# Kernel optimization log

Measured on AMD Instinct MI355X. Metric: run time of the kernel, lower is better.

The kernel has to match this reference:

```python
import jax, jax.numpy as jnp
import numpy as np

B, S, D, H = 4, 2048, 1024, 16
HD = D // H  # 64


def setup_inputs() -> dict:
    key = jax.random.key(0)
    k1, k2, k3 = jax.random.split(key, 3)
    scale = 1.0 / np.sqrt(D)
    return {
        "x": jax.random.normal(k1, (B, S, D), dtype=jnp.float32),
        "W_qkv": jax.random.normal(k2, (3 * D, D), dtype=jnp.float32) * scale,
        "b_qkv": jnp.zeros((3 * D,), dtype=jnp.float32),
        "W_out": jax.random.normal(k3, (D, D), dtype=jnp.float32) * scale,
        "b_out": jnp.zeros((D,), dtype=jnp.float32),
    }


def reference(x, W_qkv, b_qkv, W_out, b_out):
    b, s, d = x.shape
    # fused QKV projection: [b, s, 3d]
    qkv = jnp.einsum("bsd,ed->bse", x, W_qkv) + b_qkv
    # [b, s, H, 3*hd] -> [b, H, s, 3*hd]
    qkv = qkv.reshape(b, s, H, 3 * HD).transpose(0, 2, 1, 3)
    q, k, v = jnp.split(qkv, 3, axis=-1)  # each [b, H, s, hd]
    scaled = jnp.einsum("bhqd,bhkd->bhqk", q, k) / jnp.sqrt(jnp.float32(HD))
    attention = jax.nn.softmax(scaled, axis=-1)  # [b, H, s, s]
    values = jnp.einsum("bhqk,bhkd->bhqd", attention, v)
    values = values.transpose(0, 2, 1, 3).reshape(b, s, d)
    out = jnp.einsum("bsd,ed->bse", values, W_out) + b_out
    return out
```

## Files before the change

### kernel.cpp

```cpp
#include <hip/hip_runtime.h>

#define SEQ   2048
#define DM    1024
#define NHEAD 16
#define NBAT  4
#define NQKV  3072
#define MTOT  8192

typedef __attribute__((ext_vector_type(8))) short bf16x8;
typedef __attribute__((ext_vector_type(4))) float f32x4;
typedef __attribute__((ext_vector_type(16))) float f32x16;
typedef __attribute__((ext_vector_type(2))) unsigned int uint2v;

__device__ __forceinline__ unsigned short f2bf(float f) {
    union { float f; unsigned int u; } v; v.f = f;
    return (unsigned short)((v.u + 0x7FFFu + ((v.u >> 16) & 1u)) >> 16);
}

__device__ __forceinline__ void gl_lds16(const void* g, void* l) {
    __builtin_amdgcn_global_load_lds(
        (const __attribute__((address_space(1))) unsigned int*)(unsigned long long)g,
        (__attribute__((address_space(3))) unsigned int*)(unsigned int)(unsigned long long)l,
        16, 0, 0);
}

__global__ __launch_bounds__(256) void k_cvt_all(const float* __restrict__ x,
                                                 const float* __restrict__ wq,
                                                 const float* __restrict__ wo,
                                                 unsigned short* __restrict__ xb,
                                                 unsigned short* __restrict__ wqb,
                                                 unsigned short* __restrict__ wob) {
    int i = blockIdx.x * 256 + threadIdx.x;
    const float* s; unsigned short* d; int j;
    if (i < 2097152)      { s = x;  d = xb;  j = i; }
    else if (i < 2883584) { s = wq; d = wqb; j = i - 2097152; }
    else                  { s = wo; d = wob; j = i - 2883584; }
    float4 v = reinterpret_cast<const float4*>(s)[j];
    ushort4 o = { f2bf(v.x), f2bf(v.y), f2bf(v.z), f2bf(v.w) };
    reinterpret_cast<ushort4*>(d)[j] = o;
}

__global__ __launch_bounds__(256) void k_qkv(const unsigned short* __restrict__ X,
                                             const unsigned short* __restrict__ W,
                                             const float* __restrict__ bias,
                                             unsigned short* __restrict__ Qb,
                                             unsigned short* __restrict__ Kb,
                                             unsigned short* __restrict__ Vtb) {
    __shared__ short As[2][128 * 32];
    __shared__ short Bs[2][128 * 32];

    const int tid = threadIdx.x;
    const int lane = tid & 63;
    const int wid = tid >> 6;
    const int lr = lane & 15, g = lane >> 4;
    const int lb = (blockIdx.x & 7) * 192 + (blockIdx.x >> 3);
    const int bm = lb / (NQKV / 128);
    const int bn = lb % (NQKV / 128);
    const int m0 = bm * 128, n0 = bn * 128;
    const int wr = (wid >> 1) * 64, wc = (wid & 1) * 64;

    const f32x4 fz = {0.f, 0.f, 0.f, 0.f};
    f32x4 acc[4][4];
#pragma unroll
    for (int i = 0; i < 4; ++i)
#pragma unroll
        for (int j = 0; j < 4; ++j) acc[i][j] = fz;

    auto stage = [&](int buf, int kt) {
#pragma unroll
        for (int p = 0; p < 2; ++p) {
            int c = wid * 128 + p * 64 + lane;
            int r_ = c >> 2;
            int kc = (c & 3) ^ (r_ & 3);
            gl_lds16(X + (size_t)(m0 + r_) * DM + kt * 32 + kc * 8, &As[buf][c * 8]);
            gl_lds16(W + (size_t)(n0 + r_) * DM + kt * 32 + kc * 8, &Bs[buf][c * 8]);
        }
    };

    stage(0, 0);
    __syncthreads();

    for (int kt = 0; kt < 32; ++kt) {
        const int cur = kt & 1;
        if (kt + 1 < 32) stage(cur ^ 1, kt + 1);
        bf16x8 a[4], b[4];
#pragma unroll
        for (int i = 0; i < 4; ++i) {
            int ra = wr + i * 16 + lr;
            a[i] = *(const bf16x8*)&As[cur][ra * 32 + ((g ^ (ra & 3)) * 8)];
            int rb = wc + i * 16 + lr;
            b[i] = *(const bf16x8*)&Bs[cur][rb * 32 + ((g ^ (rb & 3)) * 8)];
        }
#pragma unroll
        for (int i = 0; i < 4; ++i)
#pragma unroll
            for (int j = 0; j < 4; ++j)
                acc[i][j] = __builtin_amdgcn_mfma_f32_16x16x32_bf16(a[i], b[j], acc[i][j], 0, 0, 0);
        __syncthreads();
    }

#pragma unroll
    for (int j = 0; j < 4; ++j) {
        const int col = n0 + wc + j * 16 + lr;
        const int h = col / 192;
        const int cc = col - h * 192;
        const int part = cc >> 6;
        const int hd = cc & 63;
        const float bv = bias[col];
#pragma unroll
        for (int i = 0; i < 4; ++i) {
            const int mbase = m0 + wr + i * 16 + g * 4;
            const int b_ = mbase >> 11;
            const int s_ = mbase & 2047;
            const int bh = b_ * NHEAD + h;
            if (part == 2) {
                ushort4 pk = { f2bf(acc[i][j][0] + bv), f2bf(acc[i][j][1] + bv),
                               f2bf(acc[i][j][2] + bv), f2bf(acc[i][j][3] + bv) };
                *(ushort4*)&Vtb[((size_t)bh * 64 + hd) * SEQ + s_] = pk;
            } else {
#pragma unroll
                for (int r = 0; r < 4; ++r) {
                    const size_t idx = ((size_t)bh * SEQ + s_ + r) * 64 + hd;
                    float v = acc[i][j][r] + bv;
                    if (part == 0) Qb[idx] = f2bf(v * (0.125f * 1.44269504f));
                    else           Kb[idx] = f2bf(v);
                }
            }
        }
    }
}

__global__ __launch_bounds__(256) void k_attn(const unsigned short* __restrict__ Qb,
                                              const unsigned short* __restrict__ Kb,
                                              const unsigned short* __restrict__ Vtb,
                                              unsigned short* __restrict__ Ob) {
    __shared__ short Ks[2][64 * 64];
    __shared__ short Vs[2][64 * 64];

    const int tid = threadIdx.x;
    const int lane = tid & 63;
    const int wid = tid >> 6;
    const int lb = (blockIdx.x & 7) * 128 + (blockIdx.x >> 3);
    const int bh = lb >> 4;
    const int qt = lb & 15;
    const int c = lane & 31;
    const int hi = lane >> 5;

    const unsigned short* Qh = Qb + (size_t)bh * SEQ * 64;
    const unsigned short* Kh = Kb + (size_t)bh * SEQ * 64;
    const unsigned short* Vh = Vtb + (size_t)bh * 64 * SEQ;

    const int q0 = qt * 128 + wid * 32;

    bf16x8 qf[4];
#pragma unroll
    for (int kc = 0; kc < 4; ++kc)
        qf[kc] = *(const bf16x8*)&Qh[(size_t)(q0 + c) * 64 + kc * 16 + hi * 8];

    f32x16 oacc[2];
    f32x16 lacc;
    f32x16 fz16;
#pragma unroll
    for (int r = 0; r < 16; ++r) { oacc[0][r] = 0.f; oacc[1][r] = 0.f; lacc[r] = 0.f; fz16[r] = 0.f; }

    auto stageK = [&](int buf, int kt) {
#pragma unroll
        for (int p = 0; p < 2; ++p) {
            int ci = wid * 128 + p * 64 + lane;
            int r_ = ci >> 3;
            int kc = (ci & 7) ^ (r_ & 7);
            gl_lds16(Kh + (size_t)(kt * 64 + r_) * 64 + kc * 8, &Ks[buf][ci * 8]);
        }
    };
    auto stageV = [&](int buf, int kt) {
#pragma unroll
        for (int p = 0; p < 2; ++p) {
            int ci = wid * 128 + p * 64 + lane;
            int r_ = ci >> 3;
            int kc = (ci & 7) ^ (r_ & 7);
            gl_lds16(Vh + (size_t)r_ * SEQ + kt * 64 + kc * 8, &Vs[buf][ci * 8]);
        }
    };

    stageK(0, 0);
    stageV(0, 0);
    __syncthreads();

    auto tile = [&](int cur, int kt) {
        if (kt + 1 < 32) { stageK(cur ^ 1, kt + 1); stageV(cur ^ 1, kt + 1); }

        f32x16 st[2];
        __builtin_amdgcn_s_setprio(1);
#pragma unroll
        for (int t = 0; t < 2; ++t) {
            const int row = t * 32 + c;
            bf16x8 kf0 = *(const bf16x8*)&Ks[cur][row * 64 + (((hi) ^ (row & 7)) * 8)];
            st[t] = __builtin_amdgcn_mfma_f32_32x32x16_bf16(kf0, qf[0], fz16, 0, 0, 0);
#pragma unroll
            for (int kc = 1; kc < 4; ++kc) {
                bf16x8 kf = *(const bf16x8*)&Ks[cur][row * 64 + (((kc * 2 + hi) ^ (row & 7)) * 8)];
                st[t] = __builtin_amdgcn_mfma_f32_32x32x16_bf16(kf, qf[kc], st[t], 0, 0, 0);
            }
        }
        __builtin_amdgcn_s_setprio(0);

#pragma unroll
        for (int t = 0; t < 2; ++t)
#pragma unroll
            for (int r = 0; r < 16; ++r)
                st[t][r] = __builtin_amdgcn_exp2f(st[t][r]);
#pragma unroll
        for (int r = 0; r < 16; ++r)
            lacc[r] += st[0][r] + st[1][r];

        bf16x8 pa[4];
#pragma unroll
        for (int t = 0; t < 2; ++t) {
            unsigned int qd[8];
#pragma unroll
            for (int i = 0; i < 8; ++i) {
                float lo = st[t][2 * i], hg = st[t][2 * i + 1];
                unsigned int d;
                asm("v_cvt_pk_bf16_f32 %0, %1, %2" : "=v"(d) : "v"(lo), "v"(hg));
                qd[i] = d;
            }
            uint2v s02 = __builtin_amdgcn_permlane32_swap(qd[0], qd[2], false, false);
            uint2v s13 = __builtin_amdgcn_permlane32_swap(qd[1], qd[3], false, false);
            uint2v s46 = __builtin_amdgcn_permlane32_swap(qd[4], qd[6], false, false);
            uint2v s57 = __builtin_amdgcn_permlane32_swap(qd[5], qd[7], false, false);
            union { unsigned int u[4]; bf16x8 v; } pk0, pk1;
            pk0.u[0] = s02.x; pk0.u[1] = s13.x; pk0.u[2] = s02.y; pk0.u[3] = s13.y;
            pk1.u[0] = s46.x; pk1.u[1] = s57.x; pk1.u[2] = s46.y; pk1.u[3] = s57.y;
            pa[t * 2] = pk0.v;
            pa[t * 2 + 1] = pk1.v;
        }

        __builtin_amdgcn_s_setprio(1);
#pragma unroll
        for (int nb = 0; nb < 2; ++nb) {
            const int row = nb * 32 + c;
#pragma unroll
            for (int ks = 0; ks < 4; ++ks) {
                bf16x8 vf = *(const bf16x8*)&Vs[cur][row * 64 + (((ks * 2 + hi) ^ (row & 7)) * 8)];
                oacc[nb] = __builtin_amdgcn_mfma_f32_32x32x16_bf16(pa[ks], vf, oacc[nb], 0, 0, 0);
            }
        }
        __builtin_amdgcn_s_setprio(0);

        __syncthreads();
    };

    for (int kt = 0; kt < 32; kt += 2) { tile(0, kt); tile(1, kt + 1); }

    float lred[16];
#pragma unroll
    for (int r = 0; r < 16; ++r) lred[r] = lacc[r];
#pragma unroll
    for (int s2 = 8; s2 > 0; s2 >>= 1)
#pragma unroll
        for (int r = 0; r < s2; ++r) lred[r] += lred[r + s2];
    const float l_all = lred[0] + __shfl_xor(lred[0], 32);

    const int b_ = bh >> 4, h_ = bh & 15;
    const float linv = 1.0f / l_all;
#pragma unroll
    for (int r = 0; r < 16; ++r) {
        const int qrow = (r & 3) + 8 * (r >> 2) + 4 * hi;
        const float fr = __shfl(linv, qrow);
        const size_t mrow = (size_t)b_ * SEQ + q0 + qrow;
#pragma unroll
        for (int nb = 0; nb < 2; ++nb)
            Ob[mrow * DM + h_ * 64 + nb * 32 + c] = f2bf(oacc[nb][r] * fr);
    }
}

__global__ __launch_bounds__(256) void k_out(const unsigned short* __restrict__ A,
                                             const unsigned short* __restrict__ W,
                                             const float* __restrict__ bias,
                                             float* __restrict__ O) {
    __shared__ short As[2][128 * 32];
    __shared__ short Bs[2][128 * 32];

    const int tid = threadIdx.x;
    const int lane = tid & 63;
    const int wid = tid >> 6;
    const int lr = lane & 15, g = lane >> 4;
    const int lb = (blockIdx.x & 7) * 64 + (blockIdx.x >> 3);
    const int bm = lb / (DM / 128);
    const int bn = lb % (DM / 128);
    const int m0 = bm * 128, n0 = bn * 128;
    const int wr = (wid >> 1) * 64, wc = (wid & 1) * 64;

    const f32x4 fz = {0.f, 0.f, 0.f, 0.f};
    f32x4 acc[4][4];
#pragma unroll
    for (int i = 0; i < 4; ++i)
#pragma unroll
        for (int j = 0; j < 4; ++j) acc[i][j] = fz;

    auto stage = [&](int buf, int kt) {
#pragma unroll
        for (int p = 0; p < 2; ++p) {
            int c = wid * 128 + p * 64 + lane;
            int r_ = c >> 2;
            int kc = (c & 3) ^ (r_ & 3);
            gl_lds16(A + (size_t)(m0 + r_) * DM + kt * 32 + kc * 8, &As[buf][c * 8]);
            gl_lds16(W + (size_t)(n0 + r_) * DM + kt * 32 + kc * 8, &Bs[buf][c * 8]);
        }
    };

    stage(0, 0);
    __syncthreads();

    for (int kt = 0; kt < 32; ++kt) {
        const int cur = kt & 1;
        if (kt + 1 < 32) stage(cur ^ 1, kt + 1);
        bf16x8 a[4], b[4];
#pragma unroll
        for (int i = 0; i < 4; ++i) {
            int ra = wr + i * 16 + lr;
            a[i] = *(const bf16x8*)&As[cur][ra * 32 + ((g ^ (ra & 3)) * 8)];
            int rb = wc + i * 16 + lr;
            b[i] = *(const bf16x8*)&Bs[cur][rb * 32 + ((g ^ (rb & 3)) * 8)];
        }
#pragma unroll
        for (int i = 0; i < 4; ++i)
#pragma unroll
            for (int j = 0; j < 4; ++j)
                acc[i][j] = __builtin_amdgcn_mfma_f32_16x16x32_bf16(a[i], b[j], acc[i][j], 0, 0, 0);
        __syncthreads();
    }

#pragma unroll
    for (int j = 0; j < 4; ++j) {
        const int col = n0 + wc + j * 16 + lr;
        const float bv = bias[col];
#pragma unroll
        for (int i = 0; i < 4; ++i) {
            const int mb = m0 + wr + i * 16 + g * 4;
#pragma unroll
            for (int r = 0; r < 4; ++r)
                O[(size_t)(mb + r) * DM + col] = acc[i][j][r] + bv;
        }
    }
}

extern "C" void kernel_launch(void* const* d_in, const int* in_sizes, int n_in,
                              void* d_out, int out_size, void* d_ws, size_t ws_size,
                              hipStream_t stream) {
    const float* x    = (const float*)d_in[0];
    const float* Wqkv = (const float*)d_in[1];
    const float* bqkv = (const float*)d_in[2];
    const float* Wout = (const float*)d_in[3];
    const float* bout = (const float*)d_in[4];
    float* out = (float*)d_out;

    char* ws = (char*)d_ws;
    unsigned short* xb   = (unsigned short*)(ws);
    unsigned short* wqb  = (unsigned short*)(ws + (16u << 20));
    unsigned short* wob  = (unsigned short*)(ws + (22u << 20));
    unsigned short* Qb   = (unsigned short*)(ws + (24u << 20));
    unsigned short* Kb   = (unsigned short*)(ws + (40u << 20));
    unsigned short* Vtb  = (unsigned short*)(ws + (56u << 20));
    unsigned short* valb = (unsigned short*)(ws + (72u << 20));

    k_cvt_all<<<12288, 256, 0, stream>>>(x, Wqkv, Wout, xb, wqb, wob);
    k_qkv<<<64 * 24, 256, 0, stream>>>(xb, wqb, bqkv, Qb, Kb, Vtb);
    k_attn<<<64 * 16, 256, 0, stream>>>(Qb, Kb, Vtb, valb);
    k_out<<<64 * 8, 256, 0, stream>>>(valb, wob, bout, out);
}
```

Measured before the change: 202.4 us.

## Load K and V fragments directly from global memory instead of LDS staging

Removes the double-buffered LDS staging of K and V tiles, along with the per-tile barriers, in the attention kernel. Each wave now loads its MFMA operand fragments for K and transposed V straight from global memory into registers, and the two MFMA chains are interleaved. This drops LDS traffic and synchronisation, but each of the four waves now fetches the same K/V data separately and relies on cache hits. Load latency is also no longer hidden by the prefetch of the next tile.

```diff
diff --git a/kernel.cpp b/kernel.cpp
--- a/kernel.cpp
+++ b/kernel.cpp
@@ -134,9 +134,6 @@
                                               const unsigned short* __restrict__ Kb,
                                               const unsigned short* __restrict__ Vtb,
                                               unsigned short* __restrict__ Ob) {
-    __shared__ short Ks[2][64 * 64];
-    __shared__ short Vs[2][64 * 64];
-
     const int tid = threadIdx.x;
     const int lane = tid & 63;
     const int wid = tid >> 6;
@@ -163,46 +160,35 @@
 #pragma unroll
     for (int r = 0; r < 16; ++r) { oacc[0][r] = 0.f; oacc[1][r] = 0.f; lacc[r] = 0.f; fz16[r] = 0.f; }
 
-    auto stageK = [&](int buf, int kt) {
-#pragma unroll
-        for (int p = 0; p < 2; ++p) {
-            int ci = wid * 128 + p * 64 + lane;
-            int r_ = ci >> 3;
-            int kc = (ci & 7) ^ (r_ & 7);
-            gl_lds16(Kh + (size_t)(kt * 64 + r_) * 64 + kc * 8, &Ks[buf][ci * 8]);
-        }
-    };
-    auto stageV = [&](int buf, int kt) {
-#pragma unroll
-        for (int p = 0; p < 2; ++p) {
-            int ci = wid * 128 + p * 64 + lane;
-            int r_ = ci >> 3;
-            int kc = (ci & 7) ^ (r_ & 7);
-            gl_lds16(Vh + (size_t)r_ * SEQ + kt * 64 + kc * 8, &Vs[buf][ci * 8]);
-        }
-    };
-
-    stageK(0, 0);
-    stageV(0, 0);
-    __syncthreads();
-
-    auto tile = [&](int cur, int kt) {
-        if (kt + 1 < 32) { stageK(cur ^ 1, kt + 1); stageV(cur ^ 1, kt + 1); }
+    const unsigned short* kp = Kh + (size_t)c * 64 + hi * 8;
+    const unsigned short* vp0 = Vh + (size_t)c * SEQ + hi * 8;
+    const unsigned short* vp1 = Vh + (size_t)(32 + c) * SEQ + hi * 8;
+
+    for (int kt = 0; kt < 32; ++kt) {
+        bf16x8 kf0[4], kf1[4];
+#pragma unroll
+        for (int kc = 0; kc < 4; ++kc) {
+            kf0[kc] = *(const bf16x8*)&kp[(size_t)kt * 4096 + kc * 16];
+            kf1[kc] = *(const bf16x8*)&kp[(size_t)kt * 4096 + 2048 + kc * 16];
+        }
 
         f32x16 st[2];
         __builtin_amdgcn_s_setprio(1);
-#pragma unroll
-        for (int t = 0; t < 2; ++t) {
-            const int row = t * 32 + c;
-            bf16x8 kf0 = *(const bf16x8*)&Ks[cur][row * 64 + (((hi) ^ (row & 7)) * 8)];
-            st[t] = __builtin_amdgcn_mfma_f32_32x32x16_bf16(kf0, qf[0], fz16, 0, 0, 0);
-#pragma unroll
-            for (int kc = 1; kc < 4; ++kc) {
-                bf16x8 kf = *(const bf16x8*)&Ks[cur][row * 64 + (((kc * 2 + hi) ^ (row & 7)) * 8)];
-                st[t] = __builtin_amdgcn_mfma_f32_32x32x16_bf16(kf, qf[kc], st[t], 0, 0, 0);
-            }
+        st[0] = __builtin_amdgcn_mfma_f32_32x32x16_bf16(kf0[0], qf[0], fz16, 0, 0, 0);
+        st[1] = __builtin_amdgcn_mfma_f32_32x32x16_bf16(kf1[0], qf[0], fz16, 0, 0, 0);
+#pragma unroll
+        for (int kc = 1; kc < 4; ++kc) {
+            st[0] = __builtin_amdgcn_mfma_f32_32x32x16_bf16(kf0[kc], qf[kc], st[0], 0, 0, 0);
+            st[1] = __builtin_amdgcn_mfma_f32_32x32x16_bf16(kf1[kc], qf[kc], st[1], 0, 0, 0);
         }
         __builtin_amdgcn_s_setprio(0);
+
+        bf16x8 vf0[4], vf1[4];
+#pragma unroll
+        for (int ks = 0; ks < 4; ++ks) {
+            vf0[ks] = *(const bf16x8*)&vp0[kt * 64 + ks * 16];
+            vf1[ks] = *(const bf16x8*)&vp1[kt * 64 + ks * 16];
+        }
 
 #pragma unroll
         for (int t = 0; t < 2; ++t)
@@ -237,20 +223,12 @@
 
         __builtin_amdgcn_s_setprio(1);
 #pragma unroll
-        for (int nb = 0; nb < 2; ++nb) {
-            const int row = nb * 32 + c;
-#pragma unroll
-            for (int ks = 0; ks < 4; ++ks) {
-                bf16x8 vf = *(const bf16x8*)&Vs[cur][row * 64 + (((ks * 2 + hi) ^ (row & 7)) * 8)];
-                oacc[nb] = __builtin_amdgcn_mfma_f32_32x32x16_bf16(pa[ks], vf, oacc[nb], 0, 0, 0);
-            }
+        for (int ks = 0; ks < 4; ++ks) {
+            oacc[0] = __builtin_amdgcn_mfma_f32_32x32x16_bf16(pa[ks], vf0[ks], oacc[0], 0, 0, 0);
+            oacc[1] = __builtin_amdgcn_mfma_f32_32x32x16_bf16(pa[ks], vf1[ks], oacc[1], 0, 0, 0);
         }
         __builtin_amdgcn_s_setprio(0);
-
-        __syncthreads();
-    };
-
-    for (int kt = 0; kt < 32; kt += 2) { tile(0, kt); tile(1, kt + 1); }
+    }
 
     float lred[16];
 #pragma unroll
```

Result: slower. 343.2 us (+69.6%).

## Prefetch GEMM tiles two stages ahead and hoist V fragment loads in attention

Applied to the files above, without the earlier changes.

Both projection GEMMs now issue global-to-LDS loads two k-tiles ahead. They use explicit vmcnt waits and split barriers, so the next stage is issued after fragments are read into registers rather than before the MFMAs. This is meant to hide global load latency better and to drop the trailing full __syncthreads per iteration. In the attention kernel, the V fragments are read from LDS before the exp and pack phase, so LDS latency overlaps the softmax math. The cost is higher register pressure and reliance on hand-counted vmcnt values being correct.

```diff
diff --git a/kernel.cpp b/kernel.cpp
--- a/kernel.cpp
+++ b/kernel.cpp
@@ -78,11 +78,14 @@
     };
 
     stage(0, 0);
-    __syncthreads();
+    stage(1, 1);
 
     for (int kt = 0; kt < 32; ++kt) {
         const int cur = kt & 1;
-        if (kt + 1 < 32) stage(cur ^ 1, kt + 1);
+        if (kt < 31) asm volatile("s_waitcnt vmcnt(4)" ::: "memory");
+        else         asm volatile("s_waitcnt vmcnt(0)" ::: "memory");
+        __builtin_amdgcn_s_barrier();
+
         bf16x8 a[4], b[4];
 #pragma unroll
         for (int i = 0; i < 4; ++i) {
@@ -91,12 +94,16 @@
             int rb = wc + i * 16 + lr;
             b[i] = *(const bf16x8*)&Bs[cur][rb * 32 + ((g ^ (rb & 3)) * 8)];
         }
+        asm volatile("s_waitcnt lgkmcnt(0)" ::: "memory");
+        __builtin_amdgcn_sched_barrier(0);
+        __builtin_amdgcn_s_barrier();
+        if (kt + 2 < 32) stage(cur, kt + 2);
+
 #pragma unroll
         for (int i = 0; i < 4; ++i)
 #pragma unroll
             for (int j = 0; j < 4; ++j)
                 acc[i][j] = __builtin_amdgcn_mfma_f32_16x16x32_bf16(a[i], b[j], acc[i][j], 0, 0, 0);
-        __syncthreads();
     }
 
 #pragma unroll
@@ -203,6 +210,15 @@
             }
         }
         __builtin_amdgcn_s_setprio(0);
+
+        bf16x8 vf[2][4];
+#pragma unroll
+        for (int nb = 0; nb < 2; ++nb) {
+            const int row = nb * 32 + c;
+#pragma unroll
+            for (int ks = 0; ks < 4; ++ks)
+                vf[nb][ks] = *(const bf16x8*)&Vs[cur][row * 64 + (((ks * 2 + hi) ^ (row & 7)) * 8)];
+        }
 
 #pragma unroll
         for (int t = 0; t < 2; ++t)
@@ -237,13 +253,9 @@
 
         __builtin_amdgcn_s_setprio(1);
 #pragma unroll
-        for (int nb = 0; nb < 2; ++nb) {
-            const int row = nb * 32 + c;
-#pragma unroll
-            for (int ks = 0; ks < 4; ++ks) {
-                bf16x8 vf = *(const bf16x8*)&Vs[cur][row * 64 + (((ks * 2 + hi) ^ (row & 7)) * 8)];
-                oacc[nb] = __builtin_amdgcn_mfma_f32_32x32x16_bf16(pa[ks], vf, oacc[nb], 0, 0, 0);
-            }
+        for (int ks = 0; ks < 4; ++ks) {
+            oacc[0] = __builtin_amdgcn_mfma_f32_32x32x16_bf16(pa[ks], vf[0][ks], oacc[0], 0, 0, 0);
+            oacc[1] = __builtin_amdgcn_mfma_f32_32x32x16_bf16(pa[ks], vf[1][ks], oacc[1], 0, 0, 0);
         }
         __builtin_amdgcn_s_setprio(0);
 
@@ -310,11 +322,14 @@
     };
 
     stage(0, 0);
-    __syncthreads();
+    stage(1, 1);
 
     for (int kt = 0; kt < 32; ++kt) {
         const int cur = kt & 1;
-        if (kt + 1 < 32) stage(cur ^ 1, kt + 1);
+        if (kt < 31) asm volatile("s_waitcnt vmcnt(4)" ::: "memory");
+        else         asm volatile("s_waitcnt vmcnt(0)" ::: "memory");
+        __builtin_amdgcn_s_barrier();
+
         bf16x8 a[4], b[4];
 #pragma unroll
         for (int i = 0; i < 4; ++i) {
@@ -323,12 +338,16 @@
             int rb = wc + i * 16 + lr;
             b[i] = *(const bf16x8*)&Bs[cur][rb * 32 + ((g ^ (rb & 3)) * 8)];
         }
+        asm volatile("s_waitcnt lgkmcnt(0)" ::: "memory");
+        __builtin_amdgcn_sched_barrier(0);
+        __builtin_amdgcn_s_barrier();
+        if (kt + 2 < 32) stage(cur, kt + 2);
+
 #pragma unroll
         for (int i = 0; i < 4; ++i)
 #pragma unroll
             for (int j = 0; j < 4; ++j)
                 acc[i][j] = __builtin_amdgcn_mfma_f32_16x16x32_bf16(a[i], b[j], acc[i][j], 0, 0, 0);
-        __syncthreads();
     }
 
 #pragma unroll
```

Measured after the change: 194.8 us, median of 3. 1.04x faster.
